# Kernel optimization log

Measured on AMD Instinct MI355X. Metric: run time of the kernel, lower is better.

The kernel has to match this reference:

```python
import jax, jax.numpy as jnp
import numpy as np

B, D, E, H, A = 4096, 1024, 8, 1024, 512  # batch, state_dim, num_options, num_neurons, num_actions


def setup_inputs() -> dict:
    key = jax.random.key(0)
    ks = jax.random.split(key, 16)
    s = 0.02
    return {
        "state": jax.random.normal(ks[0], (B, D), jnp.float32),
        "selected_options": jax.random.randint(ks[1], (B,), 0, E, jnp.int32),
        # option network: Linear(D,H) -> ReLU -> Linear(H,E)
        "Wo1": jax.random.normal(ks[2], (D, H), jnp.float32) * s,
        "bo1": jnp.zeros((H,), jnp.float32),
        "Wo2": jax.random.normal(ks[3], (H, E), jnp.float32) * s,
        "bo2": jnp.zeros((E,), jnp.float32),
        # E expert nets, each: Linear(D,H)+ReLU -> Linear(H,H)+ReLU -> Linear(H,A)
        "We1": jax.random.normal(ks[4], (E, D, H), jnp.float32) * s,
        "be1": jnp.zeros((E, H), jnp.float32),
        "We2": jax.random.normal(ks[5], (E, H, H), jnp.float32) * s,
        "be2": jnp.zeros((E, H), jnp.float32),
        "We3": jax.random.normal(ks[6], (E, H, A), jnp.float32) * s,
        "be3": jnp.zeros((E, A), jnp.float32),
        # termination network: Linear(D,H) -> ReLU -> Linear(H,1) -> Sigmoid
        "Wt1": jax.random.normal(ks[7], (D, H), jnp.float32) * s,
        "bt1": jnp.zeros((H,), jnp.float32),
        "Wt2": jax.random.normal(ks[8], (H, 1), jnp.float32) * s,
        "bt2": jnp.zeros((1,), jnp.float32),
    }


def reference(state, selected_options, Wo1, bo1, Wo2, bo2,
              We1, be1, We2, be2, We3, be3, Wt1, bt1, Wt2, bt2):
    # option head
    option_probs = jax.nn.softmax(jnp.maximum(state @ Wo1 + bo1, 0.0) @ Wo2 + bo2, axis=-1)

    # expert MLPs: compute all experts vectorized, then gather per-sample selected expert.
    # (the torch code loops per sample; equal action sizes so no padding is needed)
    h = jnp.maximum(jnp.einsum("bd,edh->beh", state, We1) + be1, 0.0)   # [B,E,H]
    h = jnp.maximum(jnp.einsum("beh,ehk->bek", h, We2) + be2, 0.0)      # [B,E,H]
    logits = jnp.einsum("beh,eha->bea", h, We3) + be3                   # [B,E,A]
    probs_all = jax.nn.softmax(logits, axis=-1)
    sel = selected_options[:, None, None]
    action_probs = jnp.take_along_axis(probs_all, sel, axis=1)[:, 0, :]  # [B,A]
    selected_actions = jnp.argmax(action_probs, axis=-1)

    # termination head
    termination_prob = jax.nn.sigmoid(jnp.maximum(state @ Wt1 + bt1, 0.0) @ Wt2 + bt2)

    return option_probs, action_probs, termination_prob, selected_options, selected_actions
```

## Files before the change

kernel.cpp:

```cpp
#include <hip/hip_runtime.h>
#include <hip/hip_bf16.h>

#define B_ 4096
#define D_ 1024
#define E_ 8
#define H_ 1024
#define A_ 512
#define PB 6144
#define NTT 24
#define FB_CAP 128
#define FROWS (E_ * FB_CAP)
#define KSPLIT 4
#define MARGIN 3.0e-3f

typedef __attribute__((ext_vector_type(8))) short s16x8;
typedef __attribute__((ext_vector_type(4))) float f32x4;

__device__ __forceinline__ unsigned short f2bf(float f) {
    __hip_bfloat16 h = __float2bfloat16(f);
    return *reinterpret_cast<unsigned short*>(&h);
}
__device__ __forceinline__ float bf2f(unsigned short u) {
    return __uint_as_float(((unsigned int)u) << 16);
}
__device__ __forceinline__ void gload16(const void* g, void* l) {
    __builtin_amdgcn_global_load_lds(
        (const __attribute__((address_space(1))) unsigned int*)g,
        (__attribute__((address_space(3))) unsigned int*)l, 16, 0, 0);
}

__device__ __forceinline__ int a_src_chunk(int lane) { return (((lane & 7) ^ (lane >> 3)) * 8); }

__device__ __forceinline__ int t32idx(int k, int c2) {
    return k * 64 + ((c2 + 5 * (k >> 3) + k) & 63);
}

__device__ __forceinline__ void tr_tile_128x128(const float* __restrict__ src, int Nsrc,
                                                unsigned short* __restrict__ dst,
                                                unsigned int* T32) {
    const int t = threadIdx.x;
#pragma unroll
    for (int i = 0; i < 16; ++i) {
        const int id = t + i * 256;
        const int r  = id >> 5;
        const int c4 = (id & 31) * 4;
        const float4 v = *(const float4*)&src[(size_t)r * Nsrc + c4];
        const unsigned int u0 = (unsigned)f2bf(v.x) | ((unsigned)f2bf(v.y) << 16);
        const unsigned int u1 = (unsigned)f2bf(v.z) | ((unsigned)f2bf(v.w) << 16);
        T32[t32idx(r, (c4 >> 1) + 0)] = u0;
        T32[t32idx(r, (c4 >> 1) + 1)] = u1;
    }
    __syncthreads();
#pragma unroll
    for (int q = 0; q < 8; ++q) {
        const int id = t + q * 256;
        const int n = id >> 4;
        const int L = id & 15;
        const int hi = n & 1;
        unsigned int w[4];
#pragma unroll
        for (int jj = 0; jj < 4; ++jj) {
            const int k0 = L * 8 + 2 * jj;
            const unsigned int a = T32[t32idx(k0,     n >> 1)];
            const unsigned int b = T32[t32idx(k0 + 1, n >> 1)];
            const unsigned int ha = hi ? (a >> 16) : (a & 0xffffu);
            const unsigned int hb = hi ? (b >> 16) : (b & 0xffffu);
            w[jj] = ha | (hb << 16);
        }
        *(uint4*)&dst[(size_t)n * 1024 + L * 8] = make_uint4(w[0], w[1], w[2], w[3]);
    }
}

__global__ __launch_bounds__(256)
void k_prep(const float* __restrict__ x, unsigned short* __restrict__ y,
            const float* __restrict__ Wo1, const float* __restrict__ Wt1,
            unsigned short* __restrict__ Wbf,
            const float* __restrict__ We1, unsigned short* __restrict__ We1t,
            const float* __restrict__ We2, unsigned short* __restrict__ We2t,
            const float* __restrict__ We3, unsigned short* __restrict__ We3t,
            const int* __restrict__ sel, int* __restrict__ tile_expert,
            int* __restrict__ rowlist, int* __restrict__ pos_of_row,
            int* __restrict__ rowlist2, int* __restrict__ cur2) {
    __shared__ unsigned int T32[128 * 64];
    const int t = threadIdx.x;
    const int bid = blockIdx.x;
    if (bid >= 2177) {
        const int q = bid - 2177;
        const int e = q >> 5, r = q & 31, kt = r >> 2, ntb = r & 3;
        tr_tile_128x128(We3 + (size_t)e * 524288 + (size_t)(kt * 128) * 512 + ntb * 128, 512,
                        We3t + (size_t)e * 524288 + (size_t)(ntb * 128) * 1024 + kt * 128, T32);
        return;
    }
    if (bid >= 1665) {
        const int q = bid - 1665;
        const int e = q >> 6, r = q & 63, kt = r >> 3, ntb = r & 7;
        tr_tile_128x128(We2 + (size_t)e * 1048576 + (size_t)(kt * 128) * 1024 + ntb * 128, 1024,
                        We2t + (size_t)e * 1048576 + (size_t)(ntb * 128) * 1024 + kt * 128, T32);
        return;
    }
    if (bid >= 1153) {
        const int q = bid - 1153;
        const int e = q >> 6, r = q & 63, kt = r >> 3, ntb = r & 7;
        tr_tile_128x128(We1 + (size_t)e * 1048576 + (size_t)(kt * 128) * 1024 + ntb * 128, 1024,
                        We1t + (size_t)e * 1048576 + (size_t)(ntb * 128) * 1024 + kt * 128, T32);
        return;
    }
    if (bid >= 1025) {
        const int q = bid - 1025;
        const int m = q >> 6, r = q & 63, kt = r >> 3, ntb = r & 7;
        const float* src = (m ? Wt1 : Wo1) + (size_t)(kt * 128) * 1024 + ntb * 128;
        tr_tile_128x128(src, 1024,
                        Wbf + (size_t)(m * 1024 + ntb * 128) * 1024 + kt * 128, T32);
        return;
    }
    if (bid > 0) {
        const int base = (bid - 1) * 1024 + t;
#pragma unroll
        for (int j = 0; j < 4; ++j) {
            const int i = base + j * 256;
            float4 v = ((const float4*)x)[i];
            ushort4 o;
            o.x = f2bf(v.x); o.y = f2bf(v.y); o.z = f2bf(v.z); o.w = f2bf(v.w);
            ((ushort4*)y)[i] = o;
        }
        return;
    }
    __shared__ int scnt[E_], soff[E_], scur[E_];
    if (t < E_) { scnt[t] = 0; scur[t] = 0; cur2[t] = 0; }
    for (int i = t; i < PB; i += 256) rowlist[i] = -1;
    for (int i = t; i < FROWS; i += 256) rowlist2[i] = -1;
    __syncthreads();
    for (int b = t; b < B_; b += 256) {
        int e = sel[b]; e = e < 0 ? 0 : (e >= E_ ? E_ - 1 : e);
        atomicAdd(&scnt[e], 1);
    }
    __syncthreads();
    if (t == 0) {
        int off = 0;
        for (int e = 0; e < E_; ++e) {
            soff[e] = off;
            int tiles = (scnt[e] + 255) >> 8;
            for (int k = 0; k < tiles; ++k) tile_expert[(off >> 8) + k] = e;
            off += tiles << 8;
        }
        for (int k = off >> 8; k < NTT; ++k) tile_expert[k] = -1;
    }
    __syncthreads();
    for (int b = t; b < B_; b += 256) {
        int e = sel[b]; e = e < 0 ? 0 : (e >= E_ ? E_ - 1 : e);
        int pos = atomicAdd(&scur[e], 1);
        int p = soff[e] + pos; if (p >= PB) p = PB - 1;
        rowlist[p] = b;
        pos_of_row[b] = p;
    }
}

template<int TN>
__device__ __forceinline__ void gemm3(
    const unsigned short* __restrict__ g0, const unsigned short* __restrict__ g1,
    const unsigned short* __restrict__ g2, const unsigned short* __restrict__ g3,
    const unsigned short* __restrict__ Bt, int Kg, const float* __restrict__ bp,
    unsigned short* __restrict__ Cbf, float* __restrict__ Cf, int Ncols, int relu,
    unsigned short* As, unsigned short* Bs)
{
    constexpr int NI = TN / 32;
    constexpr int BTH = TN * 64;
    constexpr int BR = TN / 64;
    const int t = threadIdx.x, lane = t & 63, w = t >> 6;
    const int wr = w >> 1, wc = w & 1;
    const int aseg = w * 2048 + lane * 8;
    const int bseg = w * (BR * 512) + lane * 8;
    const int coffb = a_src_chunk(lane);
    const unsigned short* bsrc = Bt + (size_t)(w * BR * 8 + (lane >> 3)) * Kg + coffb;

    f32x4 acc[4][NI];
#pragma unroll
    for (int i = 0; i < 4; ++i)
#pragma unroll
        for (int j = 0; j < NI; ++j)
#pragma unroll
            for (int r = 0; r < 4; ++r) acc[i][j][r] = 0.f;

#define G_STAGE(IT, BUF) {                                                   \
        const int ko_ = (IT) * 64;                                           \
        const int oa_ = (BUF) * 16384 + aseg;                                \
        gload16(g0 + ko_, As + oa_);                                         \
        gload16(g1 + ko_, As + oa_ + 512);                                   \
        gload16(g2 + ko_, As + oa_ + 1024);                                  \
        gload16(g3 + ko_, As + oa_ + 1536);                                  \
        const int ob_ = (BUF) * BTH + bseg;                                  \
        _Pragma("unroll")                                                    \
        for (int j_ = 0; j_ < BR; ++j_)                                      \
            gload16(bsrc + ko_ + (size_t)(j_ * 8) * Kg, Bs + ob_ + j_ * 512); \
    }

    G_STAGE(0, 0);
    __syncthreads();

    for (int it = 0; it < 16; ++it) {
        const int cb = it & 1;
        if (it + 1 < 16) G_STAGE(it + 1, cb ^ 1);
        __builtin_amdgcn_s_setprio(1);
#pragma unroll
        for (int kq = 0; kq < 2; ++kq) {
            const int sc = kq * 4 + (lane >> 4);
            s16x8 af[4], bfr[NI];
#pragma unroll
            for (int mi = 0; mi < 4; ++mi) {
                const int ar = wr * 64 + mi * 16 + (lane & 15);
                af[mi] = *reinterpret_cast<const s16x8*>(
                    &As[cb * 16384 + ar * 64 + ((sc ^ (ar & 7)) << 3)]);
            }
#pragma unroll
            for (int ni = 0; ni < NI; ++ni) {
                const int br = wc * (TN / 2) + ni * 16 + (lane & 15);
                bfr[ni] = *reinterpret_cast<const s16x8*>(
                    &Bs[cb * BTH + br * 64 + ((sc ^ (br & 7)) << 3)]);
            }
#pragma unroll
            for (int mi = 0; mi < 4; ++mi)
#pragma unroll
                for (int ni = 0; ni < NI; ++ni)
                    acc[mi][ni] = __builtin_amdgcn_mfma_f32_16x16x32_bf16(
                        af[mi], bfr[ni], acc[mi][ni], 0, 0, 0);
        }
        __builtin_amdgcn_s_setprio(0);
        if (it + 1 < 16) __syncthreads();
    }
#undef G_STAGE

    const int cq = lane >> 4, cr = lane & 15;
#pragma unroll
    for (int ni = 0; ni < NI; ++ni) {
        const int col_l = wc * (TN / 2) + ni * 16 + cr;
        const float bv = bp[col_l];
#pragma unroll
        for (int mi = 0; mi < 4; ++mi) {
#pragma unroll
            for (int r = 0; r < 4; ++r) {
                const int row_l = wr * 64 + mi * 16 + cq * 4 + r;
                float v = acc[mi][ni][r] + bv;
                if (relu) v = fmaxf(v, 0.f);
                const size_t idx = (size_t)row_l * Ncols + col_l;
                if (Cbf) Cbf[idx] = f2bf(v);
                if (Cf)  Cf[idx] = v;
            }
        }
    }
}

__global__ __launch_bounds__(512, 2)
void k_d2(const unsigned short* __restrict__ Sbf,
          const int* __restrict__ rowlist, const int* __restrict__ tile_expert,
          const unsigned short* __restrict__ Wbf,
          const float* __restrict__ bo1, const float* __restrict__ bt1,
          const unsigned short* __restrict__ We1t, const float* __restrict__ be1,
          unsigned short* __restrict__ hopt, unsigned short* __restrict__ hterm,
          unsigned short* __restrict__ h1) {
    __shared__ __align__(16) unsigned short SMEM[4 * 16384];
    unsigned short* As = SMEM;
    unsigned short* Bs = SMEM + 2 * 16384;
    const int bid = blockIdx.x;
    const int t = threadIdx.x, lane = t & 63, w = t >> 6;
    const int coff = a_src_chunk(lane);
    const int r0l = w * 32 + (lane >> 3);
    if (bid < 128) {
        const int nt = bid & 7, mt = bid >> 3;
        const unsigned short* g0 = Sbf + (size_t)(mt * 256 + r0l) * D_ + coff;
        const unsigned short* g1 = g0 + (size_t)8 * D_;
        const unsigned short* g2 = g0 + (size_t)16 * D_;
        const unsigned short* g3 = g0 + (size_t)24 * D_;
        int ntRow; const float* bp; unsigned short* C;
        if (nt < 4) { ntRow = nt * 256; bp = bo1 + nt * 256;
                      C = hopt + (size_t)(mt * 256) * H_ + nt * 256; }
        else { ntRow = 1024 + (nt - 4) * 256; bp = bt1 + (nt - 4) * 256;
               C = hterm + (size_t)(mt * 256) * H_ + (nt - 4) * 256; }
        gemm3<256>(g0, g1, g2, g3, Wbf + (size_t)ntRow * 1024, 1024, bp,
                   C, nullptr, H_, 1, As, Bs);
    } else {
        const int q = bid - 128, nt = q & 3, mt = q >> 2;
        const int e = tile_expert[mt]; if (e < 0) return;
        const int base = mt * 256;
        const int sub = rowlist[base]; if (sub < 0) return;
        int r0 = rowlist[base + r0l];      if (r0 < 0) r0 = sub;
        int r1 = rowlist[base + r0l + 8];  if (r1 < 0) r1 = sub;
        int r2 = rowlist[base + r0l + 16]; if (r2 < 0) r2 = sub;
        int r3 = rowlist[base + r0l + 24]; if (r3 < 0) r3 = sub;
        const unsigned short* g0 = Sbf + (size_t)r0 * D_ + coff;
        const unsigned short* g1 = Sbf + (size_t)r1 * D_ + coff;
        const unsigned short* g2 = Sbf + (size_t)r2 * D_ + coff;
        const unsigned short* g3 = Sbf + (size_t)r3 * D_ + coff;
        gemm3<256>(g0, g1, g2, g3,
                   We1t + (size_t)e * 1048576 + (size_t)(nt * 256) * 1024, 1024,
                   be1 + (size_t)e * H_ + nt * 256,
                   h1 + (size_t)(mt * 256) * H_ + nt * 256, nullptr, H_, 1, As, Bs);
    }
}

__global__ __launch_bounds__(512, 2)
void k_d3(const unsigned short* __restrict__ h1, const int* __restrict__ tile_expert,
          const unsigned short* __restrict__ We2t, const float* __restrict__ be2,
          unsigned short* __restrict__ h2) {
    __shared__ __align__(16) unsigned short SMEM[2 * 16384 + 2 * 8192];
    unsigned short* As = SMEM;
    unsigned short* Bs = SMEM + 2 * 16384;
    const int t = threadIdx.x, lane = t & 63, w = t >> 6;
    const int coff = a_src_chunk(lane);
    const int r0l = w * 32 + (lane >> 3);
    const int nt = blockIdx.x & 7, mt = blockIdx.x >> 3;
    const int e = tile_expert[mt]; if (e < 0) return;
    const unsigned short* g0 = h1 + (size_t)(mt * 256 + r0l) * H_ + coff;
    gemm3<128>(g0, g0 + (size_t)8 * H_, g0 + (size_t)16 * H_, g0 + (size_t)24 * H_,
               We2t + (size_t)e * 1048576 + (size_t)(nt * 128) * 1024, 1024,
               be2 + (size_t)e * H_ + nt * 128,
               h2 + (size_t)(mt * 256) * H_ + nt * 128, nullptr, H_, 1, As, Bs);
}

__global__ __launch_bounds__(512, 2)
void k_d5(const unsigned short* __restrict__ h2, const int* __restrict__ tile_expert,
          const unsigned short* __restrict__ We3t, const float* __restrict__ be3,
          float* __restrict__ lgt) {
    __shared__ __align__(16) unsigned short SMEM[2 * 16384 + 2 * 4096];
    unsigned short* As = SMEM;
    unsigned short* Bs = SMEM + 2 * 16384;
    const int t = threadIdx.x, lane = t & 63, w = t >> 6;
    const int coff = a_src_chunk(lane);
    const int r0l = w * 32 + (lane >> 3);
    const int nt = blockIdx.x & 7, mt = blockIdx.x >> 3;
    const int e = tile_expert[mt]; if (e < 0) return;
    const unsigned short* g0 = h2 + (size_t)(mt * 256 + r0l) * H_ + coff;
    gemm3<64>(g0, g0 + (size_t)8 * H_, g0 + (size_t)16 * H_, g0 + (size_t)24 * H_,
              We3t + (size_t)e * 524288 + (size_t)(nt * 64) * 1024, 1024,
              be3 + (size_t)e * A_ + nt * 64,
              nullptr, lgt + (size_t)(mt * 256) * A_ + nt * 64, A_, 0, As, Bs);
}

__device__ __forceinline__ void opt_body(int b, const unsigned short* __restrict__ h,
                                         const float* __restrict__ Wo2, const float* __restrict__ bo2,
                                         float* __restrict__ out, float* sm) {
    const int t = threadIdx.x;
    float acc[E_];
#pragma unroll
    for (int j = 0; j < E_; ++j) acc[j] = 0.f;
    for (int k = t; k < H_; k += 256) {
        float hv = bf2f(h[(size_t)b * H_ + k]);
#pragma unroll
        for (int j = 0; j < E_; ++j) acc[j] = fmaf(hv, Wo2[k * E_ + j], acc[j]);
    }
#pragma unroll
    for (int j = 0; j < E_; ++j)
        for (int off = 32; off; off >>= 1) acc[j] += __shfl_down(acc[j], off, 64);
    float* red = sm;
    float* probs = sm + 4 * E_;
    int wave = t >> 6, lane = t & 63;
    if (lane == 0)
        for (int j = 0; j < E_; ++j) red[wave * E_ + j] = acc[j];
    __syncthreads();
    if (t == 0) {
        float z[E_]; float m = -1e30f;
        for (int j = 0; j < E_; ++j) {
            z[j] = red[j] + red[E_ + j] + red[2 * E_ + j] + red[3 * E_ + j] + bo2[j];
            m = fmaxf(m, z[j]);
        }
        float s = 0.f;
        for (int j = 0; j < E_; ++j) { z[j] = expf(z[j] - m); s += z[j]; }
        float inv = 1.f / s;
        for (int j = 0; j < E_; ++j) probs[j] = z[j] * inv;
    }
    __syncthreads();
    if (t < E_) out[(size_t)b * E_ + t] = probs[t];
}

__device__ __forceinline__ void term_body(int b, const unsigned short* __restrict__ h,
                                          const float* __restrict__ Wt2, const float* __restrict__ bt2,
                                          float* __restrict__ out, float* sm) {
    const int t = threadIdx.x;
    float acc = 0.f;
    for (int k = t; k < H_; k += 256) acc = fmaf(bf2f(h[(size_t)b * H_ + k]), Wt2[k], acc);
    for (int off = 32; off; off >>= 1) acc += __shfl_down(acc, off, 64);
    if ((t & 63) == 0) sm[t >> 6] = acc;
    __syncthreads();
    if (t == 0) {
        float z = sm[0] + sm[1] + sm[2] + sm[3] + bt2[0];
        out[b] = 1.f / (1.f + expf(-z));
    }
}

__global__ __launch_bounds__(256)
void k_gather(const float* __restrict__ logits, const int* __restrict__ pos_of_row,
              const int* __restrict__ sel,
              float* __restrict__ out_probs, float* __restrict__ out_selopt,
              float* __restrict__ out_selact,
              int* __restrict__ rowlist2, int* __restrict__ cur2,
              const unsigned short* __restrict__ hopt, const float* __restrict__ Wo2,
              const float* __restrict__ bo2, float* __restrict__ out_opt,
              const unsigned short* __restrict__ hterm, const float* __restrict__ Wt2,
              const float* __restrict__ bt2, float* __restrict__ out_term) {
    __shared__ float smbuf[5 * E_ + 8];
    const int bid = blockIdx.x;
    if (bid >= 2 * B_) { term_body(bid - 2 * B_, hterm, Wt2, bt2, out_term, smbuf); return; }
    if (bid >= B_)     { opt_body(bid - B_, hopt, Wo2, bo2, out_opt, smbuf); return; }

    const int b = bid;
    int p = pos_of_row[b];
    if (p < 0) p = 0; if (p >= PB) p = PB - 1;
    const int t = threadIdx.x;
    const float* L = logits + (size_t)p * A_;
    float v0 = L[t], v1 = L[t + 256];

    float bv; int bi;
    if (v0 >= v1) { bv = v0; bi = t; } else { bv = v1; bi = t + 256; }
    for (int off = 32; off; off >>= 1) {
        float ov = __shfl_down(bv, off, 64);
        int   oi = __shfl_down(bi, off, 64);
        if (ov > bv || (ov == bv && oi < bi)) { bv = ov; bi = oi; }
    }
    __shared__ float rv[4]; __shared__ int ri[4];
    int wave = t >> 6, lane = t & 63;
    if (lane == 0) { rv[wave] = bv; ri[wave] = bi; }
    __syncthreads();
    __shared__ float sM; __shared__ int sBi;
    if (t == 0) {
        float mv = rv[0]; int mi = ri[0];
        for (int w = 1; w < 4; ++w)
            if (rv[w] > mv || (rv[w] == mv && ri[w] < mi)) { mv = rv[w]; mi = ri[w]; }
        sM = mv; sBi = mi;
    }
    __syncthreads();
    const float M = sM; const int BI = sBi;

    float e0 = expf(v0 - M), e1 = expf(v1 - M);
    float s = e0 + e1;
    for (int off = 32; off; off >>= 1) s += __shfl_down(s, off, 64);
    __shared__ float reds[4];
    if (lane == 0) reds[wave] = s;
    __syncthreads();
    float inv = 1.f / (reds[0] + reds[1] + reds[2] + reds[3]);

    out_probs[(size_t)b * A_ + t]       = e0 * inv;
    out_probs[(size_t)b * A_ + t + 256] = e1 * inv;

    float s0 = (t == BI) ? -1e30f : v0;
    float s1 = (t + 256 == BI) ? -1e30f : v1;
    float sm = fmaxf(s0, s1);
    for (int off = 32; off; off >>= 1) sm = fmaxf(sm, __shfl_down(sm, off, 64));
    __shared__ float red2[4];
    if (lane == 0) red2[wave] = sm;
    __syncthreads();

    if (t == 0) {
        float second = fmaxf(fmaxf(red2[0], red2[1]), fmaxf(red2[2], red2[3]));
        out_selact[b] = (float)BI;
        int e = sel[b]; e = e < 0 ? 0 : (e >= E_ ? E_ - 1 : e);
        out_selopt[b] = (float)sel[b];
        if (M - second < MARGIN) {
            int pos = atomicAdd(&cur2[e], 1);
            if (pos < FB_CAP) rowlist2[e * FB_CAP + pos] = b;
        }
    }
}

#define BM 64
#define BN 64
#define BK 32

__global__ __launch_bounds__(256)
void k_pgemm(const float* __restrict__ A, int lda, const int* __restrict__ flags,
             int gather, const float* __restrict__ W,
             float* __restrict__ P, int K, int N) {
    __shared__ float As_[BK][BM + 4];
    __shared__ float Bs_[BK][BN];

    const int mt = blockIdx.y, nt = blockIdx.x, kz = blockIdx.z;
    if (flags[mt * BM] < 0) return;
    const int e = mt >> 1;
    const float* Wb = W + (size_t)e * K * N + (size_t)nt * BN;

    const int t  = threadIdx.x;
    const int tx = t & 15;
    const int ty = t >> 4;

    const int arow = t >> 3;
    const int ak   = (t & 7) * 4;
    int r0 = mt * BM + arow, r1 = r0 + 32;
    if (gather) { r0 = flags[r0]; r1 = flags[r1]; }
    const int bkr = t >> 4;
    const int bn  = (t & 15) * 4;

    float acc[4][4];
#pragma unroll
    for (int i = 0; i < 4; ++i)
#pragma unroll
        for (int j = 0; j < 4; ++j) acc[i][j] = 0.0f;

    const int kbeg = kz * (K / KSPLIT);
    const int kend = kbeg + (K / KSPLIT);
    for (int k0 = kbeg; k0 < kend; k0 += BK) {
        float4 a0 = make_float4(0.f, 0.f, 0.f, 0.f), a1 = a0;
        if (r0 >= 0) a0 = *(const float4*)&A[(size_t)r0 * lda + k0 + ak];
        if (r1 >= 0) a1 = *(const float4*)&A[(size_t)r1 * lda + k0 + ak];
        float4 b0 = *(const float4*)&Wb[(size_t)(k0 + bkr) * N + bn];
        float4 b1 = *(const float4*)&Wb[(size_t)(k0 + bkr + 16) * N + bn];

        __syncthreads();
        As_[ak + 0][arow] = a0.x; As_[ak + 1][arow] = a0.y;
        As_[ak + 2][arow] = a0.z; As_[ak + 3][arow] = a0.w;
        As_[ak + 0][arow + 32] = a1.x; As_[ak + 1][arow + 32] = a1.y;
        As_[ak + 2][arow + 32] = a1.z; As_[ak + 3][arow + 32] = a1.w;
        *(float4*)&Bs_[bkr][bn]      = b0;
        *(float4*)&Bs_[bkr + 16][bn] = b1;
        __syncthreads();

#pragma unroll
        for (int kk = 0; kk < BK; ++kk) {
            const float4 av = *(const float4*)&As_[kk][ty * 4];
            const float4 bv = *(const float4*)&Bs_[kk][tx * 4];
            const float a_[4] = {av.x, av.y, av.z, av.w};
            const float b_[4] = {bv.x, bv.y, bv.z, bv.w};
#pragma unroll
            for (int i = 0; i < 4; ++i)
#pragma unroll
                for (int j = 0; j < 4; ++j)
                    acc[i][j] = fmaf(a_[i], b_[j], acc[i][j]);
        }
    }

    float* Pz = P + (size_t)kz * FROWS * N;
    const int n0 = nt * BN + tx * 4;
#pragma unroll
    for (int i = 0; i < 4; ++i) {
        int m = mt * BM + ty * 4 + i;
        *(float4*)&Pz[(size_t)m * N + n0] = make_float4(acc[i][0], acc[i][1], acc[i][2], acc[i][3]);
    }
}

__global__ __launch_bounds__(256)
void k_fred(const float* __restrict__ P, const int* __restrict__ flags,
            const float* __restrict__ bias, float* __restrict__ C, int N, int relu) {
    const int m = blockIdx.x;
    if (flags[m] < 0) return;
    const int e = m >> 7;
    const int t = threadIdx.x;
    if (t * 4 >= N) return;
    const size_t MN = (size_t)FROWS * N;
    const size_t base = (size_t)m * N + t * 4;
    float4 s = *(const float4*)&P[base];
#pragma unroll
    for (int z = 1; z < KSPLIT; ++z) {
        float4 p = *(const float4*)&P[(size_t)z * MN + base];
        s.x += p.x; s.y += p.y; s.z += p.z; s.w += p.w;
    }
    const float* bp = bias + (size_t)e * N + t * 4;
    s.x += bp[0]; s.y += bp[1]; s.z += bp[2]; s.w += bp[3];
    if (relu) {
        s.x = fmaxf(s.x, 0.f); s.y = fmaxf(s.y, 0.f);
        s.z = fmaxf(s.z, 0.f); s.w = fmaxf(s.w, 0.f);
    }
    *(float4*)&C[base] = s;
}

__global__ __launch_bounds__(256)
void k_fixup(const float* __restrict__ logitsf, const int* __restrict__ rowlist2,
             float* __restrict__ out_probs, float* __restrict__ out_selact) {
    const int i = blockIdx.x;
    const int row = rowlist2[i];
    if (row < 0) return;
    const int t = threadIdx.x;
    const float* L = logitsf + (size_t)i * A_;
    float v0 = L[t], v1 = L[t + 256];

    float bv; int bi;
    if (v0 >= v1) { bv = v0; bi = t; } else { bv = v1; bi = t + 256; }
    for (int off = 32; off; off >>= 1) {
        float ov = __shfl_down(bv, off, 64);
        int   oi = __shfl_down(bi, off, 64);
        if (ov > bv || (ov == bv && oi < bi)) { bv = ov; bi = oi; }
    }
    __shared__ float rv[4]; __shared__ int ri[4];
    int wave = t >> 6, lane = t & 63;
    if (lane == 0) { rv[wave] = bv; ri[wave] = bi; }
    __syncthreads();
    __shared__ float sM; __shared__ int sBi;
    if (t == 0) {
        float mv = rv[0]; int mi = ri[0];
        for (int w = 1; w < 4; ++w)
            if (rv[w] > mv || (rv[w] == mv && ri[w] < mi)) { mv = rv[w]; mi = ri[w]; }
        sM = mv; sBi = mi;
    }
    __syncthreads();

    float e0 = expf(v0 - sM), e1 = expf(v1 - sM);
    float s = e0 + e1;
    for (int off = 32; off; off >>= 1) s += __shfl_down(s, off, 64);
    __shared__ float reds[4];
    if (lane == 0) reds[wave] = s;
    __syncthreads();
    float inv = 1.f / (reds[0] + reds[1] + reds[2] + reds[3]);

    out_probs[(size_t)row * A_ + t]       = e0 * inv;
    out_probs[(size_t)row * A_ + t + 256] = e1 * inv;
    if (t == 0) out_selact[row] = (float)sBi;
}

extern "C" void kernel_launch(void* const* d_in, const int* in_sizes, int n_in,
                              void* d_out, int out_size, void* d_ws, size_t ws_size,
                              hipStream_t stream) {
    const float* state = (const float*)d_in[0];
    const int*   sel   = (const int*)d_in[1];
    const float* Wo1 = (const float*)d_in[2];
    const float* bo1 = (const float*)d_in[3];
    const float* Wo2 = (const float*)d_in[4];
    const float* bo2 = (const float*)d_in[5];
    const float* We1 = (const float*)d_in[6];
    const float* be1 = (const float*)d_in[7];
    const float* We2 = (const float*)d_in[8];
    const float* be2 = (const float*)d_in[9];
    const float* We3 = (const float*)d_in[10];
    const float* be3 = (const float*)d_in[11];
    const float* Wt1 = (const float*)d_in[12];
    const float* bt1 = (const float*)d_in[13];
    const float* Wt2 = (const float*)d_in[14];
    const float* bt2 = (const float*)d_in[15];
    float* out = (float*)d_out;

    char* w = (char*)d_ws;
    int* meta        = (int*)w;
    int* rowlist     = meta;
    int* pos_of_row  = meta + 6144;
    int* rowlist2    = meta + 10240;
    int* tile_expert = meta + 11264;
    int* cur2        = meta + 11296;
    char* P0 = w + 65536;
    char* P1 = P0 + 12582912;
    char* P2 = P1 + 16777216;
    char* W1 = P2 + 12582912;
    char* W2 = W1 + 16777216;
    char* W3 = W2 + 16777216;
    unsigned short* Sbf   = (unsigned short*)P0;
    unsigned short* Wbf   = (unsigned short*)(P0 + (8u << 20));
    unsigned short* h2b   = (unsigned short*)P0;
    unsigned short* hopt  = (unsigned short*)P1;
    unsigned short* hterm = hopt + (size_t)B_ * H_;
    unsigned short* h1b   = (unsigned short*)P2;
    unsigned short* We1t  = (unsigned short*)W1;
    unsigned short* We2t  = (unsigned short*)W2;
    unsigned short* We3t  = (unsigned short*)W3;
    float* lgt  = (float*)P2;
    float* Pbuf = (float*)P1;
    float* h1f  = (float*)P0;
    float* h2f  = h1f + (size_t)FROWS * H_;
    float* lgf  = h2f + (size_t)FROWS * H_;

    size_t act_off    = (size_t)B_ * E_;
    size_t term_off   = act_off + (size_t)B_ * A_;
    size_t selopt_off = term_off + B_;
    size_t selact_off = selopt_off + B_;

    k_prep<<<2433, 256, 0, stream>>>(state, Sbf, Wo1, Wt1, Wbf, We1, We1t,
                                     We2, We2t, We3, We3t,
                                     sel, tile_expert, rowlist, pos_of_row, rowlist2, cur2);

    k_d2<<<224, 512, 0, stream>>>(Sbf, rowlist, tile_expert, Wbf,
                                  bo1, bt1, We1t, be1, hopt, hterm, h1b);
    k_d3<<<192, 512, 0, stream>>>(h1b, tile_expert, We2t, be2, h2b);
    k_d5<<<192, 512, 0, stream>>>(h2b, tile_expert, We3t, be3, lgt);

    k_gather<<<3 * B_, 256, 0, stream>>>(lgt, pos_of_row, sel,
                                         out + act_off, out + selopt_off, out + selact_off,
                                         rowlist2, cur2,
                                         hopt, Wo2, bo2, out,
                                         hterm, Wt2, bt2, out + term_off);

    k_pgemm<<<dim3(H_ / BN, FROWS / BM, KSPLIT), 256, 0, stream>>>(state, D_, rowlist2, 1, We1, Pbuf, D_, H_);
    k_fred<<<FROWS, 256, 0, stream>>>(Pbuf, rowlist2, be1, h1f, H_, 1);
    k_pgemm<<<dim3(H_ / BN, FROWS / BM, KSPLIT), 256, 0, stream>>>(h1f, H_, rowlist2, 0, We2, Pbuf, H_, H_);
    k_fred<<<FROWS, 256, 0, stream>>>(Pbuf, rowlist2, be2, h2f, H_, 1);
    k_pgemm<<<dim3(A_ / BN, FROWS / BM, KSPLIT), 256, 0, stream>>>(h2f, H_, rowlist2, 0, We3, Pbuf, H_, A_);
    k_fred<<<FROWS, 256, 0, stream>>>(Pbuf, rowlist2, be3, lgf, A_, 0);
    k_fixup<<<FROWS, 256, 0, stream>>>(lgf, rowlist2, out + act_off, out + selact_off);
}
```

Baseline: 213.4 us.

## Overlap expert weight transposes with preceding GEMM stages

Moves the bf16 transpose of We1, We2 and We3 out of the prep kernel and into extra blocks of the GEMM kernels that run one stage earlier. The d2 kernel is split into a dense option/termination GEMM that also transposes We1, and an expert-1 GEMM that also transposes We2, while d3 transposes We3. The aim is to fill idle CUs during the small-grid GEMMs with the memory-bound conversion work instead of running it serially in the prep kernel. The cost is one extra kernel launch and transpose blocks competing with GEMM blocks for bandwidth and LDS.

```diff
diff --git a/kernel.cpp b/kernel.cpp
--- a/kernel.cpp
+++ b/kernel.cpp
@@ -71,40 +71,52 @@
     }
 }
 
+__device__ __forceinline__ void tr_tile_128x128_w512(const float* __restrict__ src, int Nsrc,
+                                                     unsigned short* __restrict__ dst,
+                                                     unsigned int* T32) {
+    const int t = threadIdx.x;
+#pragma unroll
+    for (int i = 0; i < 8; ++i) {
+        const int id = t + i * 512;
+        const int r  = id >> 5;
+        const int c4 = (id & 31) * 4;
+        const float4 v = *(const float4*)&src[(size_t)r * Nsrc + c4];
+        const unsigned int u0 = (unsigned)f2bf(v.x) | ((unsigned)f2bf(v.y) << 16);
+        const unsigned int u1 = (unsigned)f2bf(v.z) | ((unsigned)f2bf(v.w) << 16);
+        T32[t32idx(r, (c4 >> 1) + 0)] = u0;
+        T32[t32idx(r, (c4 >> 1) + 1)] = u1;
+    }
+    __syncthreads();
+#pragma unroll
+    for (int q = 0; q < 4; ++q) {
+        const int id = t + q * 512;
+        const int n = id >> 4;
+        const int L = id & 15;
+        const int hi = n & 1;
+        unsigned int w[4];
+#pragma unroll
+        for (int jj = 0; jj < 4; ++jj) {
+            const int k0 = L * 8 + 2 * jj;
+            const unsigned int a = T32[t32idx(k0,     n >> 1)];
+            const unsigned int b = T32[t32idx(k0 + 1, n >> 1)];
+            const unsigned int ha = hi ? (a >> 16) : (a & 0xffffu);
+            const unsigned int hb = hi ? (b >> 16) : (b & 0xffffu);
+            w[jj] = ha | (hb << 16);
+        }
+        *(uint4*)&dst[(size_t)n * 1024 + L * 8] = make_uint4(w[0], w[1], w[2], w[3]);
+    }
+}
+
 __global__ __launch_bounds__(256)
 void k_prep(const float* __restrict__ x, unsigned short* __restrict__ y,
             const float* __restrict__ Wo1, const float* __restrict__ Wt1,
             unsigned short* __restrict__ Wbf,
-            const float* __restrict__ We1, unsigned short* __restrict__ We1t,
-            const float* __restrict__ We2, unsigned short* __restrict__ We2t,
-            const float* __restrict__ We3, unsigned short* __restrict__ We3t,
             const int* __restrict__ sel, int* __restrict__ tile_expert,
             int* __restrict__ rowlist, int* __restrict__ pos_of_row,
             int* __restrict__ rowlist2, int* __restrict__ cur2) {
     __shared__ unsigned int T32[128 * 64];
     const int t = threadIdx.x;
     const int bid = blockIdx.x;
-    if (bid >= 2177) {
-        const int q = bid - 2177;
-        const int e = q >> 5, r = q & 31, kt = r >> 2, ntb = r & 3;
-        tr_tile_128x128(We3 + (size_t)e * 524288 + (size_t)(kt * 128) * 512 + ntb * 128, 512,
-                        We3t + (size_t)e * 524288 + (size_t)(ntb * 128) * 1024 + kt * 128, T32);
-        return;
-    }
-    if (bid >= 1665) {
-        const int q = bid - 1665;
-        const int e = q >> 6, r = q & 63, kt = r >> 3, ntb = r & 7;
-        tr_tile_128x128(We2 + (size_t)e * 1048576 + (size_t)(kt * 128) * 1024 + ntb * 128, 1024,
-                        We2t + (size_t)e * 1048576 + (size_t)(ntb * 128) * 1024 + kt * 128, T32);
-        return;
-    }
-    if (bid >= 1153) {
-        const int q = bid - 1153;
-        const int e = q >> 6, r = q & 63, kt = r >> 3, ntb = r & 7;
-        tr_tile_128x128(We1 + (size_t)e * 1048576 + (size_t)(kt * 128) * 1024 + ntb * 128, 1024,
-                        We1t + (size_t)e * 1048576 + (size_t)(ntb * 128) * 1024 + kt * 128, T32);
-        return;
-    }
     if (bid >= 1025) {
         const int q = bid - 1025;
         const int m = q >> 6, r = q & 63, kt = r >> 3, ntb = r & 7;
@@ -250,64 +262,100 @@
 }
 
 __global__ __launch_bounds__(512, 2)
-void k_d2(const unsigned short* __restrict__ Sbf,
-          const int* __restrict__ rowlist, const int* __restrict__ tile_expert,
-          const unsigned short* __restrict__ Wbf,
-          const float* __restrict__ bo1, const float* __restrict__ bt1,
-          const unsigned short* __restrict__ We1t, const float* __restrict__ be1,
-          unsigned short* __restrict__ hopt, unsigned short* __restrict__ hterm,
-          unsigned short* __restrict__ h1) {
+void k_d2a(const unsigned short* __restrict__ Sbf,
+           const unsigned short* __restrict__ Wbf,
+           const float* __restrict__ bo1, const float* __restrict__ bt1,
+           const float* __restrict__ We1, unsigned short* __restrict__ We1t,
+           unsigned short* __restrict__ hopt, unsigned short* __restrict__ hterm) {
     __shared__ __align__(16) unsigned short SMEM[4 * 16384];
     unsigned short* As = SMEM;
     unsigned short* Bs = SMEM + 2 * 16384;
     const int bid = blockIdx.x;
+    if (bid >= 128) {
+        const int q = bid - 128;
+        const int e = q >> 6, r = q & 63, kt = r >> 3, ntb = r & 7;
+        tr_tile_128x128_w512(We1 + (size_t)e * 1048576 + (size_t)(kt * 128) * 1024 + ntb * 128, 1024,
+                             We1t + (size_t)e * 1048576 + (size_t)(ntb * 128) * 1024 + kt * 128,
+                             (unsigned int*)SMEM);
+        return;
+    }
     const int t = threadIdx.x, lane = t & 63, w = t >> 6;
     const int coff = a_src_chunk(lane);
     const int r0l = w * 32 + (lane >> 3);
-    if (bid < 128) {
-        const int nt = bid & 7, mt = bid >> 3;
-        const unsigned short* g0 = Sbf + (size_t)(mt * 256 + r0l) * D_ + coff;
-        const unsigned short* g1 = g0 + (size_t)8 * D_;
-        const unsigned short* g2 = g0 + (size_t)16 * D_;
-        const unsigned short* g3 = g0 + (size_t)24 * D_;
-        int ntRow; const float* bp; unsigned short* C;
-        if (nt < 4) { ntRow = nt * 256; bp = bo1 + nt * 256;
-                      C = hopt + (size_t)(mt * 256) * H_ + nt * 256; }
-        else { ntRow = 1024 + (nt - 4) * 256; bp = bt1 + (nt - 4) * 256;
-               C = hterm + (size_t)(mt * 256) * H_ + (nt - 4) * 256; }
-        gemm3<256>(g0, g1, g2, g3, Wbf + (size_t)ntRow * 1024, 1024, bp,
-                   C, nullptr, H_, 1, As, Bs);
-    } else {
-        const int q = bid - 128, nt = q & 3, mt = q >> 2;
-        const int e = tile_expert[mt]; if (e < 0) return;
-        const int base = mt * 256;
-        const int sub = rowlist[base]; if (sub < 0) return;
-        int r0 = rowlist[base + r0l];      if (r0 < 0) r0 = sub;
-        int r1 = rowlist[base + r0l + 8];  if (r1 < 0) r1 = sub;
-        int r2 = rowlist[base + r0l + 16]; if (r2 < 0) r2 = sub;
-        int r3 = rowlist[base + r0l + 24]; if (r3 < 0) r3 = sub;
-        const unsigned short* g0 = Sbf + (size_t)r0 * D_ + coff;
-        const unsigned short* g1 = Sbf + (size_t)r1 * D_ + coff;
-        const unsigned short* g2 = Sbf + (size_t)r2 * D_ + coff;
-        const unsigned short* g3 = Sbf + (size_t)r3 * D_ + coff;
-        gemm3<256>(g0, g1, g2, g3,
-                   We1t + (size_t)e * 1048576 + (size_t)(nt * 256) * 1024, 1024,
-                   be1 + (size_t)e * H_ + nt * 256,
-                   h1 + (size_t)(mt * 256) * H_ + nt * 256, nullptr, H_, 1, As, Bs);
-    }
+    const int nt = bid & 7, mt = bid >> 3;
+    const unsigned short* g0 = Sbf + (size_t)(mt * 256 + r0l) * D_ + coff;
+    const unsigned short* g1 = g0 + (size_t)8 * D_;
+    const unsigned short* g2 = g0 + (size_t)16 * D_;
+    const unsigned short* g3 = g0 + (size_t)24 * D_;
+    int ntRow; const float* bp; unsigned short* C;
+    if (nt < 4) { ntRow = nt * 256; bp = bo1 + nt * 256;
+                  C = hopt + (size_t)(mt * 256) * H_ + nt * 256; }
+    else { ntRow = 1024 + (nt - 4) * 256; bp = bt1 + (nt - 4) * 256;
+           C = hterm + (size_t)(mt * 256) * H_ + (nt - 4) * 256; }
+    gemm3<256>(g0, g1, g2, g3, Wbf + (size_t)ntRow * 1024, 1024, bp,
+               C, nullptr, H_, 1, As, Bs);
+}
+
+__global__ __launch_bounds__(512, 2)
+void k_d2b(const unsigned short* __restrict__ Sbf,
+           const int* __restrict__ rowlist, const int* __restrict__ tile_expert,
+           const unsigned short* __restrict__ We1t, const float* __restrict__ be1,
+           const float* __restrict__ We2, unsigned short* __restrict__ We2t,
+           unsigned short* __restrict__ h1) {
+    __shared__ __align__(16) unsigned short SMEM[4 * 16384];
+    unsigned short* As = SMEM;
+    unsigned short* Bs = SMEM + 2 * 16384;
+    const int bid = blockIdx.x;
+    if (bid >= 96) {
+        const int q = bid - 96;
+        const int e = q >> 6, r = q & 63, kt = r >> 3, ntb = r & 7;
+        tr_tile_128x128_w512(We2 + (size_t)e * 1048576 + (size_t)(kt * 128) * 1024 + ntb * 128, 1024,
+                             We2t + (size_t)e * 1048576 + (size_t)(ntb * 128) * 1024 + kt * 128,
+                             (unsigned int*)SMEM);
+        return;
+    }
+    const int t = threadIdx.x, lane = t & 63, w = t >> 6;
+    const int coff = a_src_chunk(lane);
+    const int r0l = w * 32 + (lane >> 3);
+    const int nt = bid & 3, mt = bid >> 2;
+    const int e = tile_expert[mt]; if (e < 0) return;
+    const int base = mt * 256;
+    const int sub = rowlist[base]; if (sub < 0) return;
+    int r0 = rowlist[base + r0l];      if (r0 < 0) r0 = sub;
+    int r1 = rowlist[base + r0l + 8];  if (r1 < 0) r1 = sub;
+    int r2 = rowlist[base + r0l + 16]; if (r2 < 0) r2 = sub;
+    int r3 = rowlist[base + r0l + 24]; if (r3 < 0) r3 = sub;
+    const unsigned short* g0 = Sbf + (size_t)r0 * D_ + coff;
+    const unsigned short* g1 = Sbf + (size_t)r1 * D_ + coff;
+    const unsigned short* g2 = Sbf + (size_t)r2 * D_ + coff;
+    const unsigned short* g3 = Sbf + (size_t)r3 * D_ + coff;
+    gemm3<256>(g0, g1, g2, g3,
+               We1t + (size_t)e * 1048576 + (size_t)(nt * 256) * 1024, 1024,
+               be1 + (size_t)e * H_ + nt * 256,
+               h1 + (size_t)(mt * 256) * H_ + nt * 256, nullptr, H_, 1, As, Bs);
 }
 
 __global__ __launch_bounds__(512, 2)
 void k_d3(const unsigned short* __restrict__ h1, const int* __restrict__ tile_expert,
           const unsigned short* __restrict__ We2t, const float* __restrict__ be2,
+          const float* __restrict__ We3, unsigned short* __restrict__ We3t,
           unsigned short* __restrict__ h2) {
     __shared__ __align__(16) unsigned short SMEM[2 * 16384 + 2 * 8192];
     unsigned short* As = SMEM;
     unsigned short* Bs = SMEM + 2 * 16384;
+    const int bid = blockIdx.x;
+    if (bid >= 192) {
+        const int q = bid - 192;
+        const int e = q >> 5, r = q & 31, kt = r >> 2, ntb = r & 3;
+        tr_tile_128x128_w512(We3 + (size_t)e * 524288 + (size_t)(kt * 128) * 512 + ntb * 128, 512,
+                             We3t + (size_t)e * 524288 + (size_t)(ntb * 128) * 1024 + kt * 128,
+                             (unsigned int*)SMEM);
+        return;
+    }
     const int t = threadIdx.x, lane = t & 63, w = t >> 6;
     const int coff = a_src_chunk(lane);
     const int r0l = w * 32 + (lane >> 3);
-    const int nt = blockIdx.x & 7, mt = blockIdx.x >> 3;
+    const int nt = bid & 7, mt = bid >> 3;
     const int e = tile_expert[mt]; if (e < 0) return;
     const unsigned short* g0 = h1 + (size_t)(mt * 256 + r0l) * H_ + coff;
     gemm3<128>(g0, g0 + (size_t)8 * H_, g0 + (size_t)16 * H_, g0 + (size_t)24 * H_,
@@ -656,13 +704,12 @@
     size_t selopt_off = term_off + B_;
     size_t selact_off = selopt_off + B_;
 
-    k_prep<<<2433, 256, 0, stream>>>(state, Sbf, Wo1, Wt1, Wbf, We1, We1t,
-                                     We2, We2t, We3, We3t,
+    k_prep<<<1153, 256, 0, stream>>>(state, Sbf, Wo1, Wt1, Wbf,
                                      sel, tile_expert, rowlist, pos_of_row, rowlist2, cur2);
 
-    k_d2<<<224, 512, 0, stream>>>(Sbf, rowlist, tile_expert, Wbf,
-                                  bo1, bt1, We1t, be1, hopt, hterm, h1b);
-    k_d3<<<192, 512, 0, stream>>>(h1b, tile_expert, We2t, be2, h2b);
+    k_d2a<<<640, 512, 0, stream>>>(Sbf, Wbf, bo1, bt1, We1, We1t, hopt, hterm);
+    k_d2b<<<608, 512, 0, stream>>>(Sbf, rowlist, tile_expert, We1t, be1, We2, We2t, h1b);
+    k_d3<<<448, 512, 0, stream>>>(h1b, tile_expert, We2t, be2, We3, We3t, h2b);
     k_d5<<<192, 512, 0, stream>>>(h2b, tile_expert, We3t, be3, lgt);
 
     k_gather<<<3 * B_, 256, 0, stream>>>(lgt, pos_of_row, sel,
```

Result: slower. 233.5 us (+9.4%).
